# Performance work log

Hardware: AMD Instinct MI355X
Metric: run time of the kernel (lower is better)

## Reference

```python
import jax, jax.numpy as jnp
import numpy as np

N = 6144
HIDDEN = 48
HEADS = 3
HEAD = HIDDEN // HEADS


def setup_inputs() -> dict:
    key = jax.random.key(0)
    ks = jax.random.split(key, 8)
    s = 1.0 / np.sqrt(HIDDEN)
    A = (jax.random.uniform(ks[0], (N, N)) < 0.05).astype(jnp.float32)
    h = jax.random.normal(ks[1], (N, HIDDEN), dtype=jnp.float32)
    Wq = jax.random.normal(ks[2], (HIDDEN, HIDDEN), dtype=jnp.float32) * s
    Wk = jax.random.normal(ks[3], (HIDDEN, HIDDEN), dtype=jnp.float32) * s
    Wv = jax.random.normal(ks[4], (HIDDEN, HIDDEN), dtype=jnp.float32) * s
    bq = jnp.zeros((HIDDEN,), jnp.float32)
    bk = jnp.zeros((HIDDEN,), jnp.float32)
    bv = jnp.zeros((HIDDEN,), jnp.float32)
    return {"A": A, "h": h, "Wq": Wq, "bq": bq, "Wk": Wk, "bk": bk, "Wv": Wv, "bv": bv}


def reference(A, h, Wq, bq, Wk, bk, Wv, bv):
    n = h.shape[0]
    # QKV projections (torch Linear: x @ W.T + b)
    q = (h @ Wq.T + bq).reshape(n, HEADS, HEAD).transpose(1, 0, 2)  # [H,N,d]
    k = (h @ Wk.T + bk).reshape(n, HEADS, HEAD).transpose(1, 0, 2)
    v = (h @ Wv.T + bv).reshape(n, HEADS, HEAD).transpose(1, 0, 2)
    # scores = (q k^T) * A / N**(-0.5)  == (q k^T) * A * sqrt(N)  (faithful to source)
    scale = jnp.asarray(n, h.dtype) ** 0.5
    scores = jnp.einsum("hnd,hmd->hnm", q, k) * A[None, :, :] * scale
    scores = jax.nn.softmax(scores, axis=2)
    out = jnp.einsum("hnm,hmd->hnd", scores, v)  # [H,N,d]
    out = out.transpose(1, 0, 2).reshape(n, HIDDEN)
    return (out, scores)
```

## Files before the change

kernel.cpp:

```cpp
#include <hip/hip_runtime.h>
#include <math.h>

#define NN   6144
#define HID  48
#define BLK  512
#define RPB  4
#define CAP  448
#define CTOT (RPB*CAP)
#define SCALE 78.38367176906175f

typedef float vf4 __attribute__((ext_vector_type(4)));

__global__ __launch_bounds__(256)
void qkv_kernel(const float* __restrict__ h,
                const float* __restrict__ Wq, const float* __restrict__ bq,
                const float* __restrict__ Wk, const float* __restrict__ bk,
                const float* __restrict__ Wv, const float* __restrict__ bv,
                float* __restrict__ qw, float* __restrict__ kw, float* __restrict__ vw) {
    int idx = blockIdx.x * blockDim.x + threadIdx.x;
    int i = idx / HID, c = idx % HID;
    const float4* h4  = (const float4*)(h + (size_t)i * HID);
    const float4* wq4 = (const float4*)(Wq + (size_t)c * HID);
    const float4* wk4 = (const float4*)(Wk + (size_t)c * HID);
    const float4* wv4 = (const float4*)(Wv + (size_t)c * HID);
    float aq = 0.f, ak = 0.f, av = 0.f;
    #pragma unroll
    for (int r = 0; r < HID / 4; ++r) {
        float4 hv = h4[r];
        float4 q4 = wq4[r], k4 = wk4[r], v4 = wv4[r];
        aq = fmaf(hv.x, q4.x, aq); aq = fmaf(hv.y, q4.y, aq);
        aq = fmaf(hv.z, q4.z, aq); aq = fmaf(hv.w, q4.w, aq);
        ak = fmaf(hv.x, k4.x, ak); ak = fmaf(hv.y, k4.y, ak);
        ak = fmaf(hv.z, k4.z, ak); ak = fmaf(hv.w, k4.w, ak);
        av = fmaf(hv.x, v4.x, av); av = fmaf(hv.y, v4.y, av);
        av = fmaf(hv.w, v4.w, av); av = fmaf(hv.z, v4.z, av);
    }
    aq += bq[c]; ak += bk[c]; av += bv[c];
    int head = c >> 4, d = c & 15;
    size_t off = ((size_t)head * NN + i) * 16 + d;
    qw[off] = aq; kw[off] = ak; vw[off] = av;
}

__global__ __launch_bounds__(256)
void vtot_kernel(const float* __restrict__ vw, float* __restrict__ vtot) {
    int c = blockIdx.x;
    int head = c >> 4, d = c & 15;
    float s = 0.f;
    for (int j = threadIdx.x; j < NN; j += 256)
        s += vw[((size_t)head * NN + j) * 16 + d];
    #pragma unroll
    for (int o = 32; o; o >>= 1) s += __shfl_xor(s, o, 64);
    __shared__ float red[4];
    int wid = threadIdx.x >> 6, lane = threadIdx.x & 63;
    if (lane == 0) red[wid] = s;
    __syncthreads();
    if (threadIdx.x == 0) vtot[c] = red[0] + red[1] + red[2] + red[3];
}

__global__ __launch_bounds__(BLK)
void attn_kernel(const float* __restrict__ A,
                 const float* __restrict__ qw, const float* __restrict__ kw,
                 const float* __restrict__ vw, const float* __restrict__ vtot,
                 float* __restrict__ out) {
    __shared__ int   list[CTOT];
    __shared__ float sc[3][CTOT];
    __shared__ __align__(16) float qs[RPB * 48];
    __shared__ unsigned pm[RPB][BLK];
    __shared__ float wredML[8 * 12 * 2];
    __shared__ float MF[12], ZF[12], IVF[12];
    __shared__ unsigned wlo[8], whi[8];

    const int i0 = blockIdx.x * RPB;
    const int tid = threadIdx.x;
    const int wid = tid >> 6, lane = tid & 63;

    if (tid < RPB * 48) {
        int r = tid / 48, c = tid % 48;
        int hh = c >> 4, d = c & 15;
        qs[tid] = qw[((size_t)hh * NN + (i0 + r)) * 16 + d];
    }

    unsigned long long amask = 0ull;
    #pragma unroll
    for (int r = 0; r < RPB; ++r) {
        const vf4* Ar = (const vf4*)(A + (size_t)(i0 + r) * NN);
        #pragma unroll
        for (int c = 0; c < 3; ++c) {
            vf4 a4 = __builtin_nontemporal_load(&Ar[tid + c * BLK]);
            int p = r * 16 + c * 4;
            if (a4.x != 0.f) amask |= 1ull << (p + 0);
            if (a4.y != 0.f) amask |= 1ull << (p + 1);
            if (a4.z != 0.f) amask |= 1ull << (p + 2);
            if (a4.w != 0.f) amask |= 1ull << (p + 3);
        }
    }
    unsigned m0 = (unsigned)(amask & 0xFFFull);
    unsigned m1 = (unsigned)((amask >> 16) & 0xFFFull);
    unsigned m2 = (unsigned)((amask >> 32) & 0xFFFull);
    unsigned m3 = (unsigned)((amask >> 48) & 0xFFFull);
    unsigned lo = (unsigned)__popc(m0) | ((unsigned)__popc(m1) << 16);
    unsigned hi = (unsigned)__popc(m2) | ((unsigned)__popc(m3) << 16);

    unsigned ilo = lo, ihi = hi;
    #pragma unroll
    for (int o = 1; o < 64; o <<= 1) {
        unsigned plo = __shfl_up(ilo, o, 64);
        unsigned phi = __shfl_up(ihi, o, 64);
        if (lane >= o) { ilo += plo; ihi += phi; }
    }
    if (lane == 63) { wlo[wid] = ilo; whi[wid] = ihi; }
    __syncthreads();
    unsigned blo = ilo - lo, bhi = ihi - hi;
    unsigned tlo = 0, thi = 0;
    #pragma unroll
    for (int w = 0; w < 8; ++w) {
        unsigned a = wlo[w], b = whi[w];
        if (w < wid) { blo += a; bhi += b; }
        tlo += a; thi += b;
    }
    const int C0 = min((int)(tlo & 0xFFFFu), CAP), C1 = min((int)(tlo >> 16), CAP);
    const int C2 = min((int)(thi & 0xFFFFu), CAP), C3 = min((int)(thi >> 16), CAP);
    const int cum1 = C0, cum2 = C0 + C1, cum3 = cum2 + C2;
    int bs[4] = {(int)(blo & 0xFFFFu), (int)(blo >> 16),
                 (int)(bhi & 0xFFFFu), (int)(bhi >> 16)};
    int cu[5] = {0, cum1, cum2, cum3, cum3 + C3};
    unsigned mr[4] = {m0, m1, m2, m3};

    #pragma unroll
    for (int r = 0; r < RPB; ++r)
        pm[r][tid] = mr[r] | ((unsigned)bs[r] << 12);

    #pragma unroll
    for (int r = 0; r < RPB; ++r) {
        unsigned m = mr[r];
        int b = bs[r];
        while (m) {
            int p = __ffs(m) - 1; m &= m - 1;
            if (b < CAP) list[cu[r] + b] = 4 * (tid + (p >> 2) * BLK) + (p & 3);
            ++b;
        }
    }
    __syncthreads();

    {
        const int q4 = tid >> 2, part = tid & 3;
        #pragma unroll
        for (int r = 0; r < RPB; ++r) {
            float4 qv0 = ((const float4*)(qs + r * 48 +  0))[part];
            float4 qv1 = ((const float4*)(qs + r * 48 + 16))[part];
            float4 qv2 = ((const float4*)(qs + r * 48 + 32))[part];
            float mA = 0.f, lA = 0.f, mB = 0.f, lB = 0.f, mC = 0.f, lC = 0.f;
            for (int e = cu[r] + q4; e < cu[r + 1]; e += (BLK >> 2)) {
                int j = list[e];
                float4 k0 = ((const float4*)(kw + ((size_t)0 * NN + j) * 16))[part];
                float4 k1 = ((const float4*)(kw + ((size_t)1 * NN + j) * 16))[part];
                float4 k2 = ((const float4*)(kw + ((size_t)2 * NN + j) * 16))[part];
                float d0 = k0.x * qv0.x; d0 = fmaf(k0.y, qv0.y, d0);
                d0 = fmaf(k0.z, qv0.z, d0); d0 = fmaf(k0.w, qv0.w, d0);
                float d1 = k1.x * qv1.x; d1 = fmaf(k1.y, qv1.y, d1);
                d1 = fmaf(k1.z, qv1.z, d1); d1 = fmaf(k1.w, qv1.w, d1);
                float d2 = k2.x * qv2.x; d2 = fmaf(k2.y, qv2.y, d2);
                d2 = fmaf(k2.z, qv2.z, d2); d2 = fmaf(k2.w, qv2.w, d2);
                d0 += __shfl_xor(d0, 1, 64); d0 += __shfl_xor(d0, 2, 64);
                d1 += __shfl_xor(d1, 1, 64); d1 += __shfl_xor(d1, 2, 64);
                d2 += __shfl_xor(d2, 1, 64); d2 += __shfl_xor(d2, 2, 64);
                float s0 = d0 * SCALE, s1 = d1 * SCALE, s2 = d2 * SCALE;
                if (part == 0) sc[0][e] = s0;
                else if (part == 1) sc[1][e] = s1;
                else if (part == 2) sc[2][e] = s2;
                float nm;
                nm = fmaxf(mA, s0); lA = lA * __expf(mA - nm) + __expf(s0 - nm); mA = nm;
                nm = fmaxf(mB, s1); lB = lB * __expf(mB - nm) + __expf(s1 - nm); mB = nm;
                nm = fmaxf(mC, s2); lC = lC * __expf(mC - nm) + __expf(s2 - nm); mC = nm;
            }
            #pragma unroll
            for (int o = 4; o < 64; o <<= 1) {
                float om, ol, nm;
                om = __shfl_xor(mA, o, 64); ol = __shfl_xor(lA, o, 64);
                nm = fmaxf(mA, om); lA = lA * __expf(mA - nm) + ol * __expf(om - nm); mA = nm;
                om = __shfl_xor(mB, o, 64); ol = __shfl_xor(lB, o, 64);
                nm = fmaxf(mB, om); lB = lB * __expf(mB - nm) + ol * __expf(om - nm); mB = nm;
                om = __shfl_xor(mC, o, 64); ol = __shfl_xor(lC, o, 64);
                nm = fmaxf(mC, om); lC = lC * __expf(mC - nm) + ol * __expf(om - nm); mC = nm;
            }
            if (lane == 0) {
                int b0 = (wid * 12 + r * 3) * 2;
                wredML[b0 + 0] = mA; wredML[b0 + 1] = lA;
                wredML[b0 + 2] = mB; wredML[b0 + 3] = lB;
                wredML[b0 + 4] = mC; wredML[b0 + 5] = lC;
            }
        }
    }
    __syncthreads();

    if (tid < 12) {
        int r = tid / 3;
        int Cr = (r == 0) ? C0 : (r == 1) ? C1 : (r == 2) ? C2 : C3;
        float M = wredML[tid * 2], L = wredML[tid * 2 + 1];
        #pragma unroll
        for (int w = 1; w < 8; ++w) {
            float mw = wredML[(w * 12 + tid) * 2], lw = wredML[(w * 12 + tid) * 2 + 1];
            float nm = fmaxf(M, mw);
            L = L * __expf(M - nm) + lw * __expf(mw - nm);
            M = nm;
        }
        float z = __expf(-M);
        MF[tid] = M; ZF[tid] = z;
        IVF[tid] = 1.0f / (L + (float)(NN - Cr) * z);
    }
    __syncthreads();

    if (wid < 3) {
        const int h = wid, rr4 = lane & 3, a = lane >> 2;
        const float* vbase = vw + (size_t)h * NN * 16 + rr4 * 4;
        #pragma unroll
        for (int r = 0; r < RPB; ++r) {
            int s = r * 3 + h;
            float M = MF[s], zz = ZF[s], iv = IVF[s];
            float ax = 0.f, ay = 0.f, az = 0.f, aw = 0.f;
            #pragma unroll 2
            for (int e = cu[r] + a; e < cu[r + 1]; e += 16) {
                float p = __expf(sc[h][e] - M);
                float w = p - zz;
                int j = list[e];
                float4 vv = *(const float4*)(vbase + (size_t)j * 16);
                ax = fmaf(w, vv.x, ax); ay = fmaf(w, vv.y, ay);
                az = fmaf(w, vv.z, az); aw = fmaf(w, vv.w, aw);
            }
            #pragma unroll
            for (int o = 4; o < 64; o <<= 1) {
                ax += __shfl_xor(ax, o, 64); ay += __shfl_xor(ay, o, 64);
                az += __shfl_xor(az, o, 64); aw += __shfl_xor(aw, o, 64);
            }
            if (a == 0) {
                int c0 = h * 16 + rr4 * 4;
                float4 vt = *(const float4*)(vtot + c0);
                float4 o4;
                o4.x = (ax + zz * vt.x) * iv;
                o4.y = (ay + zz * vt.y) * iv;
                o4.z = (az + zz * vt.z) * iv;
                o4.w = (aw + zz * vt.w) * iv;
                *(float4*)(out + (size_t)(i0 + r) * HID + c0) = o4;
            }
        }
    } else {
        float* Pp = out + (size_t)NN * HID;
        const size_t NSQ = (size_t)NN * NN;
        const int t = tid - 192;
        #pragma unroll
        for (int r = 0; r < RPB; ++r) {
            int s = r * 3;
            float M0 = MF[s], M1 = MF[s + 1], M2 = MF[s + 2];
            float iv0 = IVF[s], iv1 = IVF[s + 1], iv2 = IVF[s + 2];
            float zi0 = ZF[s] * iv0, zi1 = ZF[s + 1] * iv1, zi2 = ZF[s + 2] * iv2;
            size_t rowoff = (size_t)(i0 + r) * NN;
            #pragma unroll 2
            for (int p = t; p < NN / 4; p += 320) {
                unsigned pk = pm[r][p & (BLK - 1)];
                int c = p >> 9;
                unsigned msk = pk & 0xFFFu;
                unsigned nib = (msk >> (c * 4)) & 0xFu;
                int idx = (int)(pk >> 12) + __popc(msk & ((1u << (c * 4)) - 1u));
                vf4 P0, P1, P2;
                #pragma unroll
                for (int e = 0; e < 4; ++e) {
                    int nz = (int)((nib >> e) & 1u);
                    if (nz && idx < CAP) {
                        int slot = cu[r] + idx;
                        P0[e] = __expf(sc[0][slot] - M0) * iv0;
                        P1[e] = __expf(sc[1][slot] - M1) * iv1;
                        P2[e] = __expf(sc[2][slot] - M2) * iv2;
                    } else { P0[e] = zi0; P1[e] = zi1; P2[e] = zi2; }
                    idx += nz;
                }
                __builtin_nontemporal_store(P0, &((vf4*)(Pp + rowoff))[p]);
                __builtin_nontemporal_store(P1, &((vf4*)(Pp + NSQ + rowoff))[p]);
                __builtin_nontemporal_store(P2, &((vf4*)(Pp + 2 * NSQ + rowoff))[p]);
            }
        }
    }
}

extern "C" void kernel_launch(void* const* d_in, const int* in_sizes, int n_in,
                              void* d_out, int out_size, void* d_ws, size_t ws_size,
                              hipStream_t stream) {
    const float* A  = (const float*)d_in[0];
    const float* h  = (const float*)d_in[1];
    const float* Wq = (const float*)d_in[2];
    const float* bq = (const float*)d_in[3];
    const float* Wk = (const float*)d_in[4];
    const float* bk = (const float*)d_in[5];
    const float* Wv = (const float*)d_in[6];
    const float* bv = (const float*)d_in[7];
    float* out = (float*)d_out;
    float* ws  = (float*)d_ws;

    float* qw   = ws;
    float* kw   = ws + (size_t)3 * NN * 16;
    float* vw   = ws + (size_t)6 * NN * 16;
    float* vtot = ws + (size_t)9 * NN * 16;

    qkv_kernel<<<(NN * HID) / 256, 256, 0, stream>>>(h, Wq, bq, Wk, bk, Wv, bv, qw, kw, vw);
    vtot_kernel<<<HID, 256, 0, stream>>>(vw, vtot);
    attn_kernel<<<NN / RPB, BLK, 0, stream>>>(A, qw, kw, vw, vtot, out);
}
```

Measured before the change: 609.4 us.

## Split dense probability write into separate grid-stride streaming kernel

The attention kernel now writes only the compact nonzero softmax probabilities, the per-row bitmask/prefix words and the fill constants to workspace. A new grid-stride kernel then expands them into the dense 3xNxN score output. The goal is to take the huge dense store stream off the latency-bound attention blocks, which ran with only five of eight waves writing, and let a full-occupancy kernel saturate write bandwidth. The cost is an extra launch plus workspace write and read traffic for the compact data and masks.

```diff
diff --git a/kernel.cpp b/kernel.cpp
--- a/kernel.cpp
+++ b/kernel.cpp
@@ -8,6 +8,7 @@
 #define CAP  448
 #define CTOT (RPB*CAP)
 #define SCALE 78.38367176906175f
+#define PGRID 2048
 
 typedef float vf4 __attribute__((ext_vector_type(4)));
 
@@ -61,11 +62,12 @@
 void attn_kernel(const float* __restrict__ A,
                  const float* __restrict__ qw, const float* __restrict__ kw,
                  const float* __restrict__ vw, const float* __restrict__ vtot,
-                 float* __restrict__ out) {
+                 float* __restrict__ out,
+                 float* __restrict__ Pc, unsigned* __restrict__ pmG,
+                 float* __restrict__ ziG) {
     __shared__ int   list[CTOT];
     __shared__ float sc[3][CTOT];
     __shared__ __align__(16) float qs[RPB * 48];
-    __shared__ unsigned pm[RPB][BLK];
     __shared__ float wredML[8 * 12 * 2];
     __shared__ float MF[12], ZF[12], IVF[12];
     __shared__ unsigned wlo[8], whi[8];
@@ -128,7 +130,8 @@
 
     #pragma unroll
     for (int r = 0; r < RPB; ++r)
-        pm[r][tid] = mr[r] | ((unsigned)bs[r] << 12);
+        __builtin_nontemporal_store(mr[r] | ((unsigned)bs[r] << 12),
+                                    &pmG[(size_t)(i0 + r) * BLK + tid]);
 
     #pragma unroll
     for (int r = 0; r < RPB; ++r) {
@@ -205,8 +208,9 @@
             M = nm;
         }
         float z = __expf(-M);
-        MF[tid] = M; ZF[tid] = z;
-        IVF[tid] = 1.0f / (L + (float)(NN - Cr) * z);
+        float iv = 1.0f / (L + (float)(NN - Cr) * z);
+        MF[tid] = M; ZF[tid] = z; IVF[tid] = iv;
+        ziG[(size_t)(i0 + r) * 3 + (tid - r * 3)] = z * iv;
     }
     __syncthreads();
 
@@ -244,40 +248,60 @@
             }
         }
     } else {
-        float* Pp = out + (size_t)NN * HID;
-        const size_t NSQ = (size_t)NN * NN;
         const int t = tid - 192;
         #pragma unroll
         for (int r = 0; r < RPB; ++r) {
             int s = r * 3;
             float M0 = MF[s], M1 = MF[s + 1], M2 = MF[s + 2];
             float iv0 = IVF[s], iv1 = IVF[s + 1], iv2 = IVF[s + 2];
-            float zi0 = ZF[s] * iv0, zi1 = ZF[s + 1] * iv1, zi2 = ZF[s + 2] * iv2;
-            size_t rowoff = (size_t)(i0 + r) * NN;
-            #pragma unroll 2
-            for (int p = t; p < NN / 4; p += 320) {
-                unsigned pk = pm[r][p & (BLK - 1)];
-                int c = p >> 9;
-                unsigned msk = pk & 0xFFFu;
-                unsigned nib = (msk >> (c * 4)) & 0xFu;
-                int idx = (int)(pk >> 12) + __popc(msk & ((1u << (c * 4)) - 1u));
-                vf4 P0, P1, P2;
-                #pragma unroll
-                for (int e = 0; e < 4; ++e) {
-                    int nz = (int)((nib >> e) & 1u);
-                    if (nz && idx < CAP) {
-                        int slot = cu[r] + idx;
-                        P0[e] = __expf(sc[0][slot] - M0) * iv0;
-                        P1[e] = __expf(sc[1][slot] - M1) * iv1;
-                        P2[e] = __expf(sc[2][slot] - M2) * iv2;
-                    } else { P0[e] = zi0; P1[e] = zi1; P2[e] = zi2; }
-                    idx += nz;
-                }
-                __builtin_nontemporal_store(P0, &((vf4*)(Pp + rowoff))[p]);
-                __builtin_nontemporal_store(P1, &((vf4*)(Pp + NSQ + rowoff))[p]);
-                __builtin_nontemporal_store(P2, &((vf4*)(Pp + 2 * NSQ + rowoff))[p]);
-            }
-        }
+            float* p0 = Pc + ((size_t)0 * NN + (i0 + r)) * CAP;
+            float* p1 = Pc + ((size_t)1 * NN + (i0 + r)) * CAP;
+            float* p2 = Pc + ((size_t)2 * NN + (i0 + r)) * CAP;
+            for (int e = cu[r] + t; e < cu[r + 1]; e += 320) {
+                int idx = e - cu[r];
+                __builtin_nontemporal_store(__expf(sc[0][e] - M0) * iv0, &p0[idx]);
+                __builtin_nontemporal_store(__expf(sc[1][e] - M1) * iv1, &p1[idx]);
+                __builtin_nontemporal_store(__expf(sc[2][e] - M2) * iv2, &p2[idx]);
+            }
+        }
+    }
+}
+
+__global__ __launch_bounds__(256)
+void pstream_kernel(const float* __restrict__ Pc, const unsigned* __restrict__ pmG,
+                    const float* __restrict__ ziG, float* __restrict__ out) {
+    float* Pp = out + (size_t)NN * HID;
+    const size_t NSQ = (size_t)NN * NN;
+    const int NP = NN / 4;
+    const unsigned total = (unsigned)NN * NP;
+    const unsigned stride = PGRID * 256;
+    for (unsigned t = blockIdx.x * 256 + threadIdx.x; t < total; t += stride) {
+        int i = (int)(t / (unsigned)NP);
+        int p = (int)(t - (unsigned)i * NP);
+        unsigned pk = pmG[(size_t)i * BLK + (p & (BLK - 1))];
+        int c = p >> 9;
+        unsigned msk = pk & 0xFFFu;
+        unsigned nib = (msk >> (c * 4)) & 0xFu;
+        int idx = (int)(pk >> 12) + __popc(msk & ((1u << (c * 4)) - 1u));
+        float zi0 = ziG[(size_t)i * 3 + 0];
+        float zi1 = ziG[(size_t)i * 3 + 1];
+        float zi2 = ziG[(size_t)i * 3 + 2];
+        const float* p0 = Pc + ((size_t)0 * NN + i) * CAP;
+        const float* p1 = Pc + ((size_t)1 * NN + i) * CAP;
+        const float* p2 = Pc + ((size_t)2 * NN + i) * CAP;
+        vf4 P0, P1, P2;
+        #pragma unroll
+        for (int e = 0; e < 4; ++e) {
+            int nz = (int)((nib >> e) & 1u);
+            if (nz && idx < CAP) {
+                P0[e] = p0[idx]; P1[e] = p1[idx]; P2[e] = p2[idx];
+            } else { P0[e] = zi0; P1[e] = zi1; P2[e] = zi2; }
+            idx += nz;
+        }
+        size_t rowoff = (size_t)i * NN;
+        __builtin_nontemporal_store(P0, &((vf4*)(Pp + rowoff))[p]);
+        __builtin_nontemporal_store(P1, &((vf4*)(Pp + NSQ + rowoff))[p]);
+        __builtin_nontemporal_store(P2, &((vf4*)(Pp + 2 * NSQ + rowoff))[p]);
     }
 }
 
@@ -296,11 +320,15 @@
     float* ws  = (float*)d_ws;
 
     float* qw   = ws;
-    float* kw   = ws + (size_t)3 * NN * 16;
-    float* vw   = ws + (size_t)6 * NN * 16;
-    float* vtot = ws + (size_t)9 * NN * 16;
+    float* kw   = qw + (size_t)3 * NN * 16;
+    float* vw   = kw + (size_t)3 * NN * 16;
+    float* vtot = vw + (size_t)3 * NN * 16;
+    float* ziG  = vtot + 64;
+    float* Pc   = ziG + (size_t)3 * NN;
+    unsigned* pmG = (unsigned*)(Pc + (size_t)3 * NN * CAP);
 
     qkv_kernel<<<(NN * HID) / 256, 256, 0, stream>>>(h, Wq, bq, Wk, bk, Wv, bv, qw, kw, vw);
     vtot_kernel<<<HID, 256, 0, stream>>>(vw, vtot);
-    attn_kernel<<<NN / RPB, BLK, 0, stream>>>(A, qw, kw, vw, vtot, out);
-}
+    attn_kernel<<<NN / RPB, BLK, 0, stream>>>(A, qw, kw, vw, vtot, out, Pc, pmG, ziG);
+    pstream_kernel<<<PGRID, 256, 0, stream>>>(Pc, pmG, ziG, out);
+}
```

Result: slower. 680.3 us (+11.6%).

## Halve attention block size and rebalance wave roles between PV and P-write

Applied to the files above, without the earlier changes.

Shrinks the attention block from 512 to 256 threads, so each thread scans 24 adjacency columns per row and keeps a 24-bit mask. The mask and prefix base are now stored in separate shared arrays because they no longer fit in one packed word. The PV accumulation for all three heads moves onto a single wave, which loops over heads, and the remaining three waves write the probability matrix. The intent is higher occupancy through smaller blocks, with launch bounds requesting 4 blocks per CU, at the cost of serializing the PV work on one wave and a smaller share of waves for the dominant P-store stream.

```diff
diff --git a/kernel.cpp b/kernel.cpp
--- a/kernel.cpp
+++ b/kernel.cpp
@@ -3,7 +3,7 @@
 
 #define NN   6144
 #define HID  48
-#define BLK  512
+#define BLK  256
 #define RPB  4
 #define CAP  448
 #define CTOT (RPB*CAP)
@@ -57,7 +57,7 @@
     if (threadIdx.x == 0) vtot[c] = red[0] + red[1] + red[2] + red[3];
 }
 
-__global__ __launch_bounds__(BLK)
+__global__ __launch_bounds__(BLK, 4)
 void attn_kernel(const float* __restrict__ A,
                  const float* __restrict__ qw, const float* __restrict__ kw,
                  const float* __restrict__ vw, const float* __restrict__ vtot,
@@ -65,10 +65,11 @@
     __shared__ int   list[CTOT];
     __shared__ float sc[3][CTOT];
     __shared__ __align__(16) float qs[RPB * 48];
-    __shared__ unsigned pm[RPB][BLK];
-    __shared__ float wredML[8 * 12 * 2];
+    __shared__ unsigned pmM[RPB][BLK];
+    __shared__ unsigned short pmB[RPB][BLK];
+    __shared__ float wredML[4 * 12 * 2];
     __shared__ float MF[12], ZF[12], IVF[12];
-    __shared__ unsigned wlo[8], whi[8];
+    __shared__ unsigned wlo[4], whi[4];
 
     const int i0 = blockIdx.x * RPB;
     const int tid = threadIdx.x;
@@ -80,26 +81,24 @@
         qs[tid] = qw[((size_t)hh * NN + (i0 + r)) * 16 + d];
     }
 
-    unsigned long long amask = 0ull;
+    unsigned mr[RPB];
     #pragma unroll
     for (int r = 0; r < RPB; ++r) {
         const vf4* Ar = (const vf4*)(A + (size_t)(i0 + r) * NN);
-        #pragma unroll
-        for (int c = 0; c < 3; ++c) {
+        unsigned mm = 0u;
+        #pragma unroll
+        for (int c = 0; c < 6; ++c) {
             vf4 a4 = __builtin_nontemporal_load(&Ar[tid + c * BLK]);
-            int p = r * 16 + c * 4;
-            if (a4.x != 0.f) amask |= 1ull << (p + 0);
-            if (a4.y != 0.f) amask |= 1ull << (p + 1);
-            if (a4.z != 0.f) amask |= 1ull << (p + 2);
-            if (a4.w != 0.f) amask |= 1ull << (p + 3);
-        }
-    }
-    unsigned m0 = (unsigned)(amask & 0xFFFull);
-    unsigned m1 = (unsigned)((amask >> 16) & 0xFFFull);
-    unsigned m2 = (unsigned)((amask >> 32) & 0xFFFull);
-    unsigned m3 = (unsigned)((amask >> 48) & 0xFFFull);
-    unsigned lo = (unsigned)__popc(m0) | ((unsigned)__popc(m1) << 16);
-    unsigned hi = (unsigned)__popc(m2) | ((unsigned)__popc(m3) << 16);
+            int p = c * 4;
+            if (a4.x != 0.f) mm |= 1u << (p + 0);
+            if (a4.y != 0.f) mm |= 1u << (p + 1);
+            if (a4.z != 0.f) mm |= 1u << (p + 2);
+            if (a4.w != 0.f) mm |= 1u << (p + 3);
+        }
+        mr[r] = mm;
+    }
+    unsigned lo = (unsigned)__popc(mr[0]) | ((unsigned)__popc(mr[1]) << 16);
+    unsigned hi = (unsigned)__popc(mr[2]) | ((unsigned)__popc(mr[3]) << 16);
 
     unsigned ilo = lo, ihi = hi;
     #pragma unroll
@@ -113,7 +112,7 @@
     unsigned blo = ilo - lo, bhi = ihi - hi;
     unsigned tlo = 0, thi = 0;
     #pragma unroll
-    for (int w = 0; w < 8; ++w) {
+    for (int w = 0; w < 4; ++w) {
         unsigned a = wlo[w], b = whi[w];
         if (w < wid) { blo += a; bhi += b; }
         tlo += a; thi += b;
@@ -124,11 +123,12 @@
     int bs[4] = {(int)(blo & 0xFFFFu), (int)(blo >> 16),
                  (int)(bhi & 0xFFFFu), (int)(bhi >> 16)};
     int cu[5] = {0, cum1, cum2, cum3, cum3 + C3};
-    unsigned mr[4] = {m0, m1, m2, m3};
-
-    #pragma unroll
-    for (int r = 0; r < RPB; ++r)
-        pm[r][tid] = mr[r] | ((unsigned)bs[r] << 12);
+
+    #pragma unroll
+    for (int r = 0; r < RPB; ++r) {
+        pmM[r][tid] = mr[r];
+        pmB[r][tid] = (unsigned short)bs[r];
+    }
 
     #pragma unroll
     for (int r = 0; r < RPB; ++r) {
@@ -198,7 +198,7 @@
         int Cr = (r == 0) ? C0 : (r == 1) ? C1 : (r == 2) ? C2 : C3;
         float M = wredML[tid * 2], L = wredML[tid * 2 + 1];
         #pragma unroll
-        for (int w = 1; w < 8; ++w) {
+        for (int w = 1; w < 4; ++w) {
             float mw = wredML[(w * 12 + tid) * 2], lw = wredML[(w * 12 + tid) * 2 + 1];
             float nm = fmaxf(M, mw);
             L = L * __expf(M - nm) + lw * __expf(mw - nm);
@@ -210,43 +210,46 @@
     }
     __syncthreads();
 
-    if (wid < 3) {
-        const int h = wid, rr4 = lane & 3, a = lane >> 2;
-        const float* vbase = vw + (size_t)h * NN * 16 + rr4 * 4;
-        #pragma unroll
-        for (int r = 0; r < RPB; ++r) {
-            int s = r * 3 + h;
-            float M = MF[s], zz = ZF[s], iv = IVF[s];
-            float ax = 0.f, ay = 0.f, az = 0.f, aw = 0.f;
-            #pragma unroll 2
-            for (int e = cu[r] + a; e < cu[r + 1]; e += 16) {
-                float p = __expf(sc[h][e] - M);
-                float w = p - zz;
-                int j = list[e];
-                float4 vv = *(const float4*)(vbase + (size_t)j * 16);
-                ax = fmaf(w, vv.x, ax); ay = fmaf(w, vv.y, ay);
-                az = fmaf(w, vv.z, az); aw = fmaf(w, vv.w, aw);
-            }
+    if (wid == 0) {
+        const int rr4 = lane & 3, a = lane >> 2;
+        #pragma unroll
+        for (int h = 0; h < 3; ++h) {
+            const float* vbase = vw + (size_t)h * NN * 16 + rr4 * 4;
             #pragma unroll
-            for (int o = 4; o < 64; o <<= 1) {
-                ax += __shfl_xor(ax, o, 64); ay += __shfl_xor(ay, o, 64);
-                az += __shfl_xor(az, o, 64); aw += __shfl_xor(aw, o, 64);
-            }
-            if (a == 0) {
-                int c0 = h * 16 + rr4 * 4;
-                float4 vt = *(const float4*)(vtot + c0);
-                float4 o4;
-                o4.x = (ax + zz * vt.x) * iv;
-                o4.y = (ay + zz * vt.y) * iv;
-                o4.z = (az + zz * vt.z) * iv;
-                o4.w = (aw + zz * vt.w) * iv;
-                *(float4*)(out + (size_t)(i0 + r) * HID + c0) = o4;
+            for (int r = 0; r < RPB; ++r) {
+                int s = r * 3 + h;
+                float M = MF[s], zz = ZF[s], iv = IVF[s];
+                float ax = 0.f, ay = 0.f, az = 0.f, aw = 0.f;
+                #pragma unroll 2
+                for (int e = cu[r] + a; e < cu[r + 1]; e += 16) {
+                    float p = __expf(sc[h][e] - M);
+                    float w = p - zz;
+                    int j = list[e];
+                    float4 vv = *(const float4*)(vbase + (size_t)j * 16);
+                    ax = fmaf(w, vv.x, ax); ay = fmaf(w, vv.y, ay);
+                    az = fmaf(w, vv.z, az); aw = fmaf(w, vv.w, aw);
+                }
+                #pragma unroll
+                for (int o = 4; o < 64; o <<= 1) {
+                    ax += __shfl_xor(ax, o, 64); ay += __shfl_xor(ay, o, 64);
+                    az += __shfl_xor(az, o, 64); aw += __shfl_xor(aw, o, 64);
+                }
+                if (a == 0) {
+                    int c0 = h * 16 + rr4 * 4;
+                    float4 vt = *(const float4*)(vtot + c0);
+                    float4 o4;
+                    o4.x = (ax + zz * vt.x) * iv;
+                    o4.y = (ay + zz * vt.y) * iv;
+                    o4.z = (az + zz * vt.z) * iv;
+                    o4.w = (aw + zz * vt.w) * iv;
+                    *(float4*)(out + (size_t)(i0 + r) * HID + c0) = o4;
+                }
             }
         }
     } else {
         float* Pp = out + (size_t)NN * HID;
         const size_t NSQ = (size_t)NN * NN;
-        const int t = tid - 192;
+        const int t = tid - 64;
         #pragma unroll
         for (int r = 0; r < RPB; ++r) {
             int s = r * 3;
@@ -255,12 +258,11 @@
             float zi0 = ZF[s] * iv0, zi1 = ZF[s + 1] * iv1, zi2 = ZF[s + 2] * iv2;
             size_t rowoff = (size_t)(i0 + r) * NN;
             #pragma unroll 2
-            for (int p = t; p < NN / 4; p += 320) {
-                unsigned pk = pm[r][p & (BLK - 1)];
-                int c = p >> 9;
-                unsigned msk = pk & 0xFFFu;
+            for (int p = t; p < NN / 4; p += 192) {
+                unsigned msk = pmM[r][p & (BLK - 1)];
+                int c = p >> 8;
                 unsigned nib = (msk >> (c * 4)) & 0xFu;
-                int idx = (int)(pk >> 12) + __popc(msk & ((1u << (c * 4)) - 1u));
+                int idx = (int)pmB[r][p & (BLK - 1)] + __popc(msk & ((1u << (c * 4)) - 1u));
                 vf4 P0, P1, P2;
                 #pragma unroll
                 for (int e = 0; e < 4; ++e) {
```

Measured after the change: 624.9 us. 2.5% more time.

## Fuse PV accumulation into online-softmax pass and write probabilities from all threads

Applied to the files above, without the earlier changes.

The score pass now also loads V rows and keeps flash-style running accumulators for the weighted V sum and the plain V sum, so the separate PV pass over the neighbour list is gone. Per-wave partials are merged through shared memory by 192 threads that write the output rows directly. The dense probability store now uses all 512 threads with each thread's own in-register mask instead of 320 threads reading a packed shared-memory mask. In exchange there are many more shuffles and registers in the fused loop, which may lower occupancy.

```diff
diff --git a/kernel.cpp b/kernel.cpp
--- a/kernel.cpp
+++ b/kernel.cpp
@@ -65,8 +65,9 @@
     __shared__ int   list[CTOT];
     __shared__ float sc[3][CTOT];
     __shared__ __align__(16) float qs[RPB * 48];
-    __shared__ unsigned pm[RPB][BLK];
-    __shared__ float wredML[8 * 12 * 2];
+    __shared__ float wML[8 * 12 * 2];
+    __shared__ float wAC[8 * 12 * 16];
+    __shared__ float wVS[8 * 12 * 16];
     __shared__ float MF[12], ZF[12], IVF[12];
     __shared__ unsigned wlo[8], whi[8];
 
@@ -127,10 +128,6 @@
     unsigned mr[4] = {m0, m1, m2, m3};
 
     #pragma unroll
-    for (int r = 0; r < RPB; ++r)
-        pm[r][tid] = mr[r] | ((unsigned)bs[r] << 12);
-
-    #pragma unroll
     for (int r = 0; r < RPB; ++r) {
         unsigned m = mr[r];
         int b = bs[r];
@@ -150,11 +147,16 @@
             float4 qv1 = ((const float4*)(qs + r * 48 + 16))[part];
             float4 qv2 = ((const float4*)(qs + r * 48 + 32))[part];
             float mA = 0.f, lA = 0.f, mB = 0.f, lB = 0.f, mC = 0.f, lC = 0.f;
+            vf4 ac0 = {0.f,0.f,0.f,0.f}, ac1 = {0.f,0.f,0.f,0.f}, ac2 = {0.f,0.f,0.f,0.f};
+            vf4 vs0 = {0.f,0.f,0.f,0.f}, vs1 = {0.f,0.f,0.f,0.f}, vs2 = {0.f,0.f,0.f,0.f};
             for (int e = cu[r] + q4; e < cu[r + 1]; e += (BLK >> 2)) {
                 int j = list[e];
-                float4 k0 = ((const float4*)(kw + ((size_t)0 * NN + j) * 16))[part];
-                float4 k1 = ((const float4*)(kw + ((size_t)1 * NN + j) * 16))[part];
-                float4 k2 = ((const float4*)(kw + ((size_t)2 * NN + j) * 16))[part];
+                vf4 k0 = ((const vf4*)(kw + ((size_t)0 * NN + j) * 16))[part];
+                vf4 k1 = ((const vf4*)(kw + ((size_t)1 * NN + j) * 16))[part];
+                vf4 k2 = ((const vf4*)(kw + ((size_t)2 * NN + j) * 16))[part];
+                vf4 v0 = ((const vf4*)(vw + ((size_t)0 * NN + j) * 16))[part];
+                vf4 v1 = ((const vf4*)(vw + ((size_t)1 * NN + j) * 16))[part];
+                vf4 v2 = ((const vf4*)(vw + ((size_t)2 * NN + j) * 16))[part];
                 float d0 = k0.x * qv0.x; d0 = fmaf(k0.y, qv0.y, d0);
                 d0 = fmaf(k0.z, qv0.z, d0); d0 = fmaf(k0.w, qv0.w, d0);
                 float d1 = k1.x * qv1.x; d1 = fmaf(k1.y, qv1.y, d1);
@@ -168,115 +170,136 @@
                 if (part == 0) sc[0][e] = s0;
                 else if (part == 1) sc[1][e] = s1;
                 else if (part == 2) sc[2][e] = s2;
-                float nm;
-                nm = fmaxf(mA, s0); lA = lA * __expf(mA - nm) + __expf(s0 - nm); mA = nm;
-                nm = fmaxf(mB, s1); lB = lB * __expf(mB - nm) + __expf(s1 - nm); mB = nm;
-                nm = fmaxf(mC, s2); lC = lC * __expf(mC - nm) + __expf(s2 - nm); mC = nm;
-            }
+                if (s0 > mA) {
+                    float rs = __expf(mA - s0);
+                    lA *= rs; ac0 = ac0 * rs; mA = s0;
+                }
+                float p0 = __expf(s0 - mA); lA += p0;
+                ac0.x = fmaf(p0, v0.x, ac0.x); ac0.y = fmaf(p0, v0.y, ac0.y);
+                ac0.z = fmaf(p0, v0.z, ac0.z); ac0.w = fmaf(p0, v0.w, ac0.w);
+                vs0 = vs0 + v0;
+                if (s1 > mB) {
+                    float rs = __expf(mB - s1);
+                    lB *= rs; ac1 = ac1 * rs; mB = s1;
+                }
+                float p1 = __expf(s1 - mB); lB += p1;
+                ac1.x = fmaf(p1, v1.x, ac1.x); ac1.y = fmaf(p1, v1.y, ac1.y);
+                ac1.z = fmaf(p1, v1.z, ac1.z); ac1.w = fmaf(p1, v1.w, ac1.w);
+                vs1 = vs1 + v1;
+                if (s2 > mC) {
+                    float rs = __expf(mC - s2);
+                    lC *= rs; ac2 = ac2 * rs; mC = s2;
+                }
+                float p2 = __expf(s2 - mC); lC += p2;
+                ac2.x = fmaf(p2, v2.x, ac2.x); ac2.y = fmaf(p2, v2.y, ac2.y);
+                ac2.z = fmaf(p2, v2.z, ac2.z); ac2.w = fmaf(p2, v2.w, ac2.w);
+                vs2 = vs2 + v2;
+            }
+            float MA = mA, MB = mB, MC = mC;
             #pragma unroll
             for (int o = 4; o < 64; o <<= 1) {
-                float om, ol, nm;
-                om = __shfl_xor(mA, o, 64); ol = __shfl_xor(lA, o, 64);
-                nm = fmaxf(mA, om); lA = lA * __expf(mA - nm) + ol * __expf(om - nm); mA = nm;
-                om = __shfl_xor(mB, o, 64); ol = __shfl_xor(lB, o, 64);
-                nm = fmaxf(mB, om); lB = lB * __expf(mB - nm) + ol * __expf(om - nm); mB = nm;
-                om = __shfl_xor(mC, o, 64); ol = __shfl_xor(lC, o, 64);
-                nm = fmaxf(mC, om); lC = lC * __expf(mC - nm) + ol * __expf(om - nm); mC = nm;
-            }
-            if (lane == 0) {
-                int b0 = (wid * 12 + r * 3) * 2;
-                wredML[b0 + 0] = mA; wredML[b0 + 1] = lA;
-                wredML[b0 + 2] = mB; wredML[b0 + 3] = lB;
-                wredML[b0 + 4] = mC; wredML[b0 + 5] = lC;
-            }
-        }
-    }
-    __syncthreads();
-
-    if (tid < 12) {
-        int r = tid / 3;
-        int Cr = (r == 0) ? C0 : (r == 1) ? C1 : (r == 2) ? C2 : C3;
-        float M = wredML[tid * 2], L = wredML[tid * 2 + 1];
-        #pragma unroll
-        for (int w = 1; w < 8; ++w) {
-            float mw = wredML[(w * 12 + tid) * 2], lw = wredML[(w * 12 + tid) * 2 + 1];
-            float nm = fmaxf(M, mw);
-            L = L * __expf(M - nm) + lw * __expf(mw - nm);
-            M = nm;
-        }
-        float z = __expf(-M);
-        MF[tid] = M; ZF[tid] = z;
-        IVF[tid] = 1.0f / (L + (float)(NN - Cr) * z);
-    }
-    __syncthreads();
-
-    if (wid < 3) {
-        const int h = wid, rr4 = lane & 3, a = lane >> 2;
-        const float* vbase = vw + (size_t)h * NN * 16 + rr4 * 4;
-        #pragma unroll
-        for (int r = 0; r < RPB; ++r) {
-            int s = r * 3 + h;
-            float M = MF[s], zz = ZF[s], iv = IVF[s];
-            float ax = 0.f, ay = 0.f, az = 0.f, aw = 0.f;
-            #pragma unroll 2
-            for (int e = cu[r] + a; e < cu[r + 1]; e += 16) {
-                float p = __expf(sc[h][e] - M);
-                float w = p - zz;
-                int j = list[e];
-                float4 vv = *(const float4*)(vbase + (size_t)j * 16);
-                ax = fmaf(w, vv.x, ax); ay = fmaf(w, vv.y, ay);
-                az = fmaf(w, vv.z, az); aw = fmaf(w, vv.w, aw);
-            }
+                MA = fmaxf(MA, __shfl_xor(MA, o, 64));
+                MB = fmaxf(MB, __shfl_xor(MB, o, 64));
+                MC = fmaxf(MC, __shfl_xor(MC, o, 64));
+            }
+            float rA = __expf(mA - MA), rB = __expf(mB - MB), rC = __expf(mC - MC);
+            lA *= rA; lB *= rB; lC *= rC;
+            ac0 = ac0 * rA; ac1 = ac1 * rB; ac2 = ac2 * rC;
             #pragma unroll
             for (int o = 4; o < 64; o <<= 1) {
-                ax += __shfl_xor(ax, o, 64); ay += __shfl_xor(ay, o, 64);
-                az += __shfl_xor(az, o, 64); aw += __shfl_xor(aw, o, 64);
-            }
-            if (a == 0) {
-                int c0 = h * 16 + rr4 * 4;
-                float4 vt = *(const float4*)(vtot + c0);
-                float4 o4;
-                o4.x = (ax + zz * vt.x) * iv;
-                o4.y = (ay + zz * vt.y) * iv;
-                o4.z = (az + zz * vt.z) * iv;
-                o4.w = (aw + zz * vt.w) * iv;
-                *(float4*)(out + (size_t)(i0 + r) * HID + c0) = o4;
-            }
-        }
-    } else {
-        float* Pp = out + (size_t)NN * HID;
-        const size_t NSQ = (size_t)NN * NN;
-        const int t = tid - 192;
-        #pragma unroll
-        for (int r = 0; r < RPB; ++r) {
-            int s = r * 3;
-            float M0 = MF[s], M1 = MF[s + 1], M2 = MF[s + 2];
-            float iv0 = IVF[s], iv1 = IVF[s + 1], iv2 = IVF[s + 2];
-            float zi0 = ZF[s] * iv0, zi1 = ZF[s + 1] * iv1, zi2 = ZF[s + 2] * iv2;
-            size_t rowoff = (size_t)(i0 + r) * NN;
-            #pragma unroll 2
-            for (int p = t; p < NN / 4; p += 320) {
-                unsigned pk = pm[r][p & (BLK - 1)];
-                int c = p >> 9;
-                unsigned msk = pk & 0xFFFu;
-                unsigned nib = (msk >> (c * 4)) & 0xFu;
-                int idx = (int)(pk >> 12) + __popc(msk & ((1u << (c * 4)) - 1u));
-                vf4 P0, P1, P2;
-                #pragma unroll
-                for (int e = 0; e < 4; ++e) {
-                    int nz = (int)((nib >> e) & 1u);
-                    if (nz && idx < CAP) {
-                        int slot = cu[r] + idx;
-                        P0[e] = __expf(sc[0][slot] - M0) * iv0;
-                        P1[e] = __expf(sc[1][slot] - M1) * iv1;
-                        P2[e] = __expf(sc[2][slot] - M2) * iv2;
-                    } else { P0[e] = zi0; P1[e] = zi1; P2[e] = zi2; }
-                    idx += nz;
+                lA += __shfl_xor(lA, o, 64);
+                lB += __shfl_xor(lB, o, 64);
+                lC += __shfl_xor(lC, o, 64);
+                ac0.x += __shfl_xor(ac0.x, o, 64); ac0.y += __shfl_xor(ac0.y, o, 64);
+                ac0.z += __shfl_xor(ac0.z, o, 64); ac0.w += __shfl_xor(ac0.w, o, 64);
+                ac1.x += __shfl_xor(ac1.x, o, 64); ac1.y += __shfl_xor(ac1.y, o, 64);
+                ac1.z += __shfl_xor(ac1.z, o, 64); ac1.w += __shfl_xor(ac1.w, o, 64);
+                ac2.x += __shfl_xor(ac2.x, o, 64); ac2.y += __shfl_xor(ac2.y, o, 64);
+                ac2.z += __shfl_xor(ac2.z, o, 64); ac2.w += __shfl_xor(ac2.w, o, 64);
+                vs0.x += __shfl_xor(vs0.x, o, 64); vs0.y += __shfl_xor(vs0.y, o, 64);
+                vs0.z += __shfl_xor(vs0.z, o, 64); vs0.w += __shfl_xor(vs0.w, o, 64);
+                vs1.x += __shfl_xor(vs1.x, o, 64); vs1.y += __shfl_xor(vs1.y, o, 64);
+                vs1.z += __shfl_xor(vs1.z, o, 64); vs1.w += __shfl_xor(vs1.w, o, 64);
+                vs2.x += __shfl_xor(vs2.x, o, 64); vs2.y += __shfl_xor(vs2.y, o, 64);
+                vs2.z += __shfl_xor(vs2.z, o, 64); vs2.w += __shfl_xor(vs2.w, o, 64);
+            }
+            if (lane < 4) {
+                int b = wid * 12 + r * 3;
+                if (lane == 0) {
+                    wML[(b + 0) * 2] = MA; wML[(b + 0) * 2 + 1] = lA;
+                    wML[(b + 1) * 2] = MB; wML[(b + 1) * 2 + 1] = lB;
+                    wML[(b + 2) * 2] = MC; wML[(b + 2) * 2 + 1] = lC;
                 }
-                __builtin_nontemporal_store(P0, &((vf4*)(Pp + rowoff))[p]);
-                __builtin_nontemporal_store(P1, &((vf4*)(Pp + NSQ + rowoff))[p]);
-                __builtin_nontemporal_store(P2, &((vf4*)(Pp + 2 * NSQ + rowoff))[p]);
-            }
+                int da = lane * 4;
+                wAC[(b + 0) * 16 + da + 0] = ac0.x; wAC[(b + 0) * 16 + da + 1] = ac0.y;
+                wAC[(b + 0) * 16 + da + 2] = ac0.z; wAC[(b + 0) * 16 + da + 3] = ac0.w;
+                wAC[(b + 1) * 16 + da + 0] = ac1.x; wAC[(b + 1) * 16 + da + 1] = ac1.y;
+                wAC[(b + 1) * 16 + da + 2] = ac1.z; wAC[(b + 1) * 16 + da + 3] = ac1.w;
+                wAC[(b + 2) * 16 + da + 0] = ac2.x; wAC[(b + 2) * 16 + da + 1] = ac2.y;
+                wAC[(b + 2) * 16 + da + 2] = ac2.z; wAC[(b + 2) * 16 + da + 3] = ac2.w;
+                wVS[(b + 0) * 16 + da + 0] = vs0.x; wVS[(b + 0) * 16 + da + 1] = vs0.y;
+                wVS[(b + 0) * 16 + da + 2] = vs0.z; wVS[(b + 0) * 16 + da + 3] = vs0.w;
+                wVS[(b + 1) * 16 + da + 0] = vs1.x; wVS[(b + 1) * 16 + da + 1] = vs1.y;
+                wVS[(b + 1) * 16 + da + 2] = vs1.z; wVS[(b + 1) * 16 + da + 3] = vs1.w;
+                wVS[(b + 2) * 16 + da + 0] = vs2.x; wVS[(b + 2) * 16 + da + 1] = vs2.y;
+                wVS[(b + 2) * 16 + da + 2] = vs2.z; wVS[(b + 2) * 16 + da + 3] = vs2.w;
+            }
+        }
+    }
+    __syncthreads();
+
+    if (tid < 192) {
+        int rh = tid >> 4, d = tid & 15;
+        int r = rh / 3, hh = rh - 3 * r;
+        float M = wML[rh * 2];
+        #pragma unroll
+        for (int w = 1; w < 8; ++w) M = fmaxf(M, wML[(w * 12 + rh) * 2]);
+        float L = 0.f, Acc = 0.f, VS = 0.f;
+        #pragma unroll
+        for (int w = 0; w < 8; ++w) {
+            float ew = __expf(wML[(w * 12 + rh) * 2] - M);
+            L   += wML[(w * 12 + rh) * 2 + 1] * ew;
+            Acc += wAC[(w * 12 + rh) * 16 + d] * ew;
+            VS  += wVS[(w * 12 + rh) * 16 + d];
+        }
+        int Cr = (r == 0) ? C0 : (r == 1) ? C1 : (r == 2) ? C2 : C3;
+        float z = __expf(-M);
+        float iv = 1.0f / (L + (float)(NN - Cr) * z);
+        int c = hh * 16 + d;
+        out[(size_t)(i0 + r) * HID + c] = (Acc + z * (vtot[c] - VS)) * iv;
+        if (d == 0) { MF[rh] = M; ZF[rh] = z; IVF[rh] = iv; }
+    }
+    __syncthreads();
+
+    float* Pp = out + (size_t)NN * HID;
+    const size_t NSQ = (size_t)NN * NN;
+    #pragma unroll
+    for (int r = 0; r < RPB; ++r) {
+        int s = r * 3;
+        float M0 = MF[s], M1 = MF[s + 1], M2 = MF[s + 2];
+        float iv0 = IVF[s], iv1 = IVF[s + 1], iv2 = IVF[s + 2];
+        float zi0 = ZF[s] * iv0, zi1 = ZF[s + 1] * iv1, zi2 = ZF[s + 2] * iv2;
+        size_t rowoff = (size_t)(i0 + r) * NN;
+        unsigned msk = mr[r];
+        #pragma unroll
+        for (int c = 0; c < 3; ++c) {
+            unsigned nib = (msk >> (c * 4)) & 0xFu;
+            int idx = bs[r] + __popc(msk & ((1u << (c * 4)) - 1u));
+            vf4 P0, P1, P2;
+            #pragma unroll
+            for (int e = 0; e < 4; ++e) {
+                int nz = (int)((nib >> e) & 1u);
+                if (nz && idx < CAP) {
+                    int slot = cu[r] + idx;
+                    P0[e] = __expf(sc[0][slot] - M0) * iv0;
+                    P1[e] = __expf(sc[1][slot] - M1) * iv1;
+                    P2[e] = __expf(sc[2][slot] - M2) * iv2;
+                } else { P0[e] = zi0; P1[e] = zi1; P2[e] = zi2; }
+                idx += nz;
+            }
+            __builtin_nontemporal_store(P0, &((vf4*)(Pp + rowoff))[tid + c * BLK]);
+            __builtin_nontemporal_store(P1, &((vf4*)(Pp + NSQ + rowoff))[tid + c * BLK]);
+            __builtin_nontemporal_store(P2, &((vf4*)(Pp + 2 * NSQ + rowoff))[tid + c * BLK]);
         }
     }
 }
```

Result: slower. 624.4 us (+2.5%).
